# Kernel optimization log

Hardware: AMD Instinct MI355X
Metric: run time of the kernel (lower is better)

Reference implementation:

```python
import jax, jax.numpy as jnp
import numpy as np

B, D, L, H = 4, 1024, 2048, 8
HD = D // H


def setup_inputs() -> dict:
    key = jax.random.key(0)
    k1, k2, k3, k4 = jax.random.split(key, 4)
    query = jax.random.normal(k1, (B, D, L), dtype=jnp.float32)
    mask = jax.random.randint(k2, (B, L), 0, 2, dtype=jnp.int32)
    W1 = jax.random.normal(k3, (2 * D, D), dtype=jnp.float32) * (D ** -0.5)
    Wq = jax.random.normal(k4, (D, D), dtype=jnp.float32) * (D ** -0.5)
    return {"query": query, "mask": mask, "W1": W1, "Wq": Wq}


def _split_heads(x):
    # [B, L, C] -> [B, H, L, C//H]
    b, l, c = x.shape
    return x.reshape(b, l, H, c // H).transpose(0, 2, 1, 3)


def reference(query, mask, W1, Wq):
    # 1x1 conv == channel GEMM; produce [B, L, out]
    temp = jnp.einsum('od,bdl->blo', W1, query)   # [B, L, 2D] (K|V)
    q = jnp.einsum('od,bdl->blo', Wq, query)      # [B, L, D]
    k, v = jnp.split(temp, 2, axis=-1)
    q = _split_heads(q) * (HD ** -0.5)            # [B, H, L, HD]
    k = _split_heads(k)
    v = _split_heads(v)
    scores = jnp.einsum('bhqd,bhkd->bhqk', q, k)  # [B, H, L, L]
    m = mask.astype(jnp.float32)[:, None, None, :]
    logits = scores + (-1e30) * (1.0 - m)
    weights = jax.nn.softmax(logits, axis=-1)     # dropout p=0 (eval)
    out = jnp.einsum('bhqk,bhkd->bhqd', weights, v)
    out = out.transpose(0, 2, 1, 3).reshape(B, L, D)  # merge heads
    return out.transpose(0, 2, 1)                 # [B, D, L]
```

## Files before the change

### kernel.cpp

```cpp
#include <hip/hip_runtime.h>
#include <hip/hip_bf16.h>

#define B_  4
#define D_  1024
#define L_  2048
#define H_  8
#define HD_ 128

typedef __attribute__((ext_vector_type(8))) short bf16x8;
typedef __attribute__((ext_vector_type(4))) float f32x4;
typedef __attribute__((ext_vector_type(2))) unsigned uint2v;
typedef __attribute__((ext_vector_type(4))) unsigned uint4v;

#if __has_builtin(__builtin_amdgcn_permlane16_swap) && __has_builtin(__builtin_amdgcn_permlane32_swap)
#define HAS_PERMSWAP 1
#else
#define HAS_PERMSWAP 0
#endif

static __device__ __forceinline__ ushort f2bf(float f) {
    unsigned u = __float_as_uint(f);
    unsigned r = (u + 0x7fffu + ((u >> 16) & 1u)) >> 16;
    return (ushort)r;
}

static __device__ __forceinline__ unsigned cvt_pk_bf16(float lo, float hi) {
    unsigned r;
    asm("v_cvt_pk_bf16_f32 %0, %1, %2" : "=v"(r) : "v"(lo), "v"(hi));
    return r;
}

static __device__ __forceinline__ float exp2_fast(float x) {
#if __has_builtin(__builtin_amdgcn_exp2f)
    return __builtin_amdgcn_exp2f(x);
#else
    return exp2f(x);
#endif
}

static __device__ __forceinline__ float qmax4(float x) {
#if HAS_PERMSWAP
    uint2v a = __builtin_amdgcn_permlane16_swap(__float_as_uint(x), __float_as_uint(x), false, false);
    float y = fmaxf(__uint_as_float(a[0]), __uint_as_float(a[1]));
    uint2v b = __builtin_amdgcn_permlane32_swap(__float_as_uint(y), __float_as_uint(y), false, false);
    return fmaxf(__uint_as_float(b[0]), __uint_as_float(b[1]));
#else
    x = fmaxf(x, __shfl_xor(x, 16, 64));
    return fmaxf(x, __shfl_xor(x, 32, 64));
#endif
}

static __device__ __forceinline__ void dma16(const ushort* g, ushort* l) {
    __builtin_amdgcn_global_load_lds(
        (const __attribute__((address_space(1))) void*)g,
        (__attribute__((address_space(3))) void*)l, 16, 0, 0);
}

__global__ void k_zero_out(float* __restrict__ out, int n) {
    int i = blockIdx.x * 256 + threadIdx.x;
    if (i < n) out[i] = 0.f;
}

__global__ void k_prep(const float* __restrict__ q, const float* __restrict__ W1,
                       const float* __restrict__ Wq, const int* __restrict__ mask,
                       ushort* __restrict__ Wb, ushort* __restrict__ Xt,
                       int* __restrict__ cidx, int* __restrict__ cnt) {
    __shared__ float tile[64][65];
    const int bid = blockIdx.x, t = threadIdx.x;
    if (bid < 4) {
        int b = bid;
        if (t < 64) {
            int lane = t;
            const int* mb = mask + b * L_;
            int base = 0;
            for (int c = 0; c < L_; c += 64) {
                int m = mb[c + lane];
                unsigned long long bal = __ballot(m != 0);
                int pre = __popcll(bal & ((1ull << lane) - 1ull));
                if (m) cidx[b * L_ + base + pre] = c + lane;
                base += __popcll(bal);
            }
            for (int j = base + lane; j < L_; j += 64) cidx[b * L_ + j] = 0;
            if (lane == 0) cnt[b] = base;
        }
    } else if (bid < 4 + 2048) {
        int tb = bid - 4;
        int bx = tb & 31, by = (tb >> 5) & 15, bz = tb >> 9;
        int l0 = bx * 64, d0 = by * 64;
        int rr = t >> 4, cc = t & 15;
        const float* src = q + (size_t)bz * D_ * L_;
        for (int i = 0; i < 4; i++) {
            int r = rr + 16 * i;
            float4 v = *(const float4*)&src[(size_t)(d0 + r) * L_ + l0 + cc * 4];
            tile[r][cc * 4 + 0] = v.x;
            tile[r][cc * 4 + 1] = v.y;
            tile[r][cc * 4 + 2] = v.z;
            tile[r][cc * 4 + 3] = v.w;
        }
        __syncthreads();
        ushort* dst = Xt + (size_t)bz * L_ * D_;
        for (int i = 0; i < 4; i++) {
            int lr = rr + 16 * i;
            uint2 o;
            o.x = cvt_pk_bf16(tile[cc * 4 + 0][lr], tile[cc * 4 + 1][lr]);
            o.y = cvt_pk_bf16(tile[cc * 4 + 2][lr], tile[cc * 4 + 3][lr]);
            *(uint2*)&dst[(size_t)(l0 + lr) * D_ + d0 + cc * 4] = o;
        }
    } else {
        int i = (bid - 2052) * 256 + t;
        const int n1 = 2 * D_ * D_ / 4;
        float4 v = (i < n1) ? ((const float4*)W1)[i] : ((const float4*)Wq)[i - n1];
        ushort4 o;
        o.x = f2bf(v.x); o.y = f2bf(v.y); o.z = f2bf(v.z); o.w = f2bf(v.w);
        ((ushort4*)Wb)[i] = o;
    }
}

__launch_bounds__(256)
__global__ void k_proj(const ushort* __restrict__ Wb, const ushort* __restrict__ Xt,
                       const int* __restrict__ cidx, const int* __restrict__ cnt,
                       ushort* __restrict__ Qb, ushort* __restrict__ Kb,
                       ushort* __restrict__ Vt) {
    __shared__ alignas(16) ushort As[128 * 64];
    __shared__ alignas(16) ushort Bs[128 * 64];
    const int bid = blockIdx.x;
    const int xcd = bid & 7, j = bid >> 3;
    const int wid = xcd * 192 + j;
    const int st = wid >> 4, m = wid & 15;
    const int b  = st / 24;
    const int sr = st % 24;
    const int sx = sr & 3, sy = sr >> 2;
    const int x  = sx * 4 + (m & 3);
    const int y  = sy * 4 + (m >> 2);
    const int o0 = y * 128;
    const int l0 = x * 128;
    const int type = o0 >> 10;
    if (type < 2) {
        int tiles = (cnt[b] + 127) >> 7;
        if (x >= tiles) return;
    }
    const int t = threadIdx.x;
    const int wave = t >> 6, lane = t & 63, quad = lane >> 4, li = lane & 15;
    const int wm = wave >> 1, wn = wave & 1;
    const ushort* Xb = Xt + (size_t)b * L_ * D_;

    const int srow = t >> 3;
    const int g = (t & 7) ^ (srow & 7);
    const ushort* aSrc[4];
    const ushort* bSrc[4];
    for (int i = 0; i < 4; i++) {
        int r = i * 32 + srow;
        aSrc[i] = Wb + (size_t)(o0 + r) * D_ + g * 8;
        int l = l0 + r;
        int gl = (type < 2) ? cidx[b * L_ + l] : l;
        bSrc[i] = Xb + (size_t)gl * D_ + g * 8;
    }

    f32x4 acc[4][4] = {};

    for (int k0 = 0; k0 < D_; k0 += 64) {
        for (int i = 0; i < 4; i++)
            dma16(aSrc[i] + k0, &As[(i * 256 + wave * 64) * 8]);
        for (int i = 0; i < 4; i++)
            dma16(bSrc[i] + k0, &Bs[(i * 256 + wave * 64) * 8]);
        __syncthreads();
        for (int ks = 0; ks < 64; ks += 32) {
            const int kc = ks >> 3;
            bf16x8 af[4], bfr[4];
            for (int mf = 0; mf < 4; mf++) {
                int row = wm * 64 + mf * 16 + li;
                af[mf] = *(const bf16x8*)&As[row * 64 + (((kc + quad) ^ (li & 7)) * 8)];
            }
            for (int nf = 0; nf < 4; nf++) {
                int row = wn * 64 + nf * 16 + li;
                bfr[nf] = *(const bf16x8*)&Bs[row * 64 + (((kc + quad) ^ (li & 7)) * 8)];
            }
            for (int mf = 0; mf < 4; mf++)
                for (int nf = 0; nf < 4; nf++)
                    acc[mf][nf] = __builtin_amdgcn_mfma_f32_16x16x32_bf16(af[mf], bfr[nf], acc[mf][nf], 0, 0, 0);
        }
        __syncthreads();
    }

    const float qscale = 0.1275174495450826f;
    for (int mf = 0; mf < 4; mf++) {
        int o = o0 + wm * 64 + mf * 16 + quad * 4;
        int c = o & 1023;
        int h = c >> 7, hd = c & 127;
        for (int nf = 0; nf < 4; nf++) {
            int l = l0 + wn * 64 + nf * 16 + li;
            f32x4 v = acc[mf][nf];
            if (type == 0) {
                uint2 kk;
                kk.x = cvt_pk_bf16(v[0], v[1]);
                kk.y = cvt_pk_bf16(v[2], v[3]);
                *(uint2*)&Kb[(((size_t)(b * H_ + h)) * L_ + l) * HD_ + hd] = kk;
            } else if (type == 1) {
                size_t base = (size_t)(b * H_ + h) * HD_;
                Vt[(base + hd + 0) * L_ + l] = f2bf(v[0]);
                Vt[(base + hd + 1) * L_ + l] = f2bf(v[1]);
                Vt[(base + hd + 2) * L_ + l] = f2bf(v[2]);
                Vt[(base + hd + 3) * L_ + l] = f2bf(v[3]);
            } else {
                uint2 qq;
                qq.x = cvt_pk_bf16(v[0] * qscale, v[1] * qscale);
                qq.y = cvt_pk_bf16(v[2] * qscale, v[3] * qscale);
                *(uint2*)&Qb[(((size_t)(b * H_ + h)) * L_ + l) * HD_ + hd] = qq;
            }
        }
    }
}

__launch_bounds__(256, 4)
__global__ void k_attn(const ushort* __restrict__ Qb, const ushort* __restrict__ Kb,
                       const ushort* __restrict__ Vt, const int* __restrict__ mask,
                       float* __restrict__ out) {
    __shared__ alignas(16) ushort Ks[2][32][128];
    __shared__ alignas(16) ushort Vs[2][128][32];
#if !HAS_PERMSWAP
    __shared__ alignas(16) ushort Pl[4][16][40];
#endif
    const int blk = blockIdx.x;
    const int h = blk & 7, qt = (blk >> 3) & 31, b = blk >> 8;
    const int t = threadIdx.x;
    const int w = t >> 6, lane = t & 63, quad = lane >> 4, li = lane & 15;
    const int q0 = qt * 64 + w * 16;
    const ushort* Qh = Qb + (size_t)(b * H_ + h) * L_ * HD_;
    const ushort* Kh = Kb + (size_t)(b * H_ + h) * L_ * HD_;
    const ushort* Vh = Vt + (size_t)(b * H_ + h) * HD_ * L_;
    const int* mb = mask + b * L_;

    int cm = 0;
    for (int c = lane; c < L_; c += 64) cm += mb[c];
    cm += __shfl_xor(cm, 32, 64);
    cm += __shfl_xor(cm, 16, 64);
    cm += __shfl_xor(cm, 8, 64);
    cm += __shfl_xor(cm, 4, 64);
    cm += __shfl_xor(cm, 2, 64);
    cm += __shfl_xor(cm, 1, 64);
    const int cnt = cm;
    int cnt_pad = (cnt + 31) & ~31;
    if (cnt_pad < 32) cnt_pad = 32;

    const ushort* kgp[2]; const ushort* vgp[2];
    for (int i = 0; i < 2; i++) {
        int seg = w * 2 + i;
        int key = seg * 4 + (lane >> 4);
        int ck  = (lane & 15) ^ (key & 15);
        kgp[i] = Kh + (size_t)key * HD_ + ck * 8;
        int hd  = seg * 16 + (lane >> 2);
        int cv  = (lane & 3) ^ (hd & 3);
        vgp[i] = Vh + (size_t)hd * L_ + cv * 8;
    }

    for (int i = 0; i < 2; i++) dma16(kgp[i], &Ks[0][0][0] + (w * 2 + i) * 512);
    for (int i = 0; i < 2; i++) dma16(vgp[i], &Vs[0][0][0] + (w * 2 + i) * 512);

    bf16x8 qf[4];
    for (int kf = 0; kf < 4; kf++)
        qf[kf] = *(const bf16x8*)&Qh[(size_t)(q0 + li) * HD_ + kf * 32 + quad * 8];

    bf16x8 ones;
    for (int i = 0; i < 8; i++) ones[i] = (short)0x3F80;

    float mrun = -1e30f;
    f32x4 lsum = {};
    f32x4 acc[8] = {};

    int buf = 0;
    for (int n0 = 0; n0 < cnt_pad; n0 += 32, buf ^= 1) {
        __syncthreads();

        if (n0 + 32 < cnt_pad) {
            int nb = buf ^ 1;
            for (int i = 0; i < 2; i++)
                dma16(kgp[i] + (size_t)(n0 + 32) * HD_, &Ks[nb][0][0] + (w * 2 + i) * 512);
            for (int i = 0; i < 2; i++)
                dma16(vgp[i] + (n0 + 32), &Vs[nb][0][0] + (w * 2 + i) * 512);
        }

        f32x4 s[2] = {};
        for (int kf = 0; kf < 4; kf++) {
            bf16x8 kfr[2];
            for (int mt = 0; mt < 2; mt++)
                kfr[mt] = *(const bf16x8*)&Ks[buf][mt * 16 + li][((kf * 4 + quad) ^ li) * 8];
            for (int mt = 0; mt < 2; mt++)
                s[mt] = __builtin_amdgcn_mfma_f32_16x16x32_bf16(kfr[mt], qf[kf], s[mt], 0, 0, 0);
        }

        if (n0 + 32 > cnt) {
            for (int mt = 0; mt < 2; mt++)
                for (int r = 0; r < 4; r++)
                    if (n0 + mt * 16 + quad * 4 + r >= cnt) s[mt][r] = -1e30f;
        }

        float a0 = fmaxf(fmaxf(s[0][0], s[0][1]), fmaxf(s[0][2], s[0][3]));
        float a1 = fmaxf(fmaxf(s[1][0], s[1][1]), fmaxf(s[1][2], s[1][3]));
        float nm = qmax4(fmaxf(a0, a1));
        float mnew = fmaxf(mrun, nm);
        float alpha = exp2_fast(mrun - mnew);
        mrun = mnew;
        for (int mt = 0; mt < 2; mt++)
            for (int r = 0; r < 4; r++)
                s[mt][r] = exp2_fast(s[mt][r] - mnew);

        if (__any(alpha != 1.0f)) {
            int sb = (lane & 48) | (quad * 4);
            float ar0 = __shfl(alpha, sb + 0, 64);
            float ar1 = __shfl(alpha, sb + 1, 64);
            float ar2 = __shfl(alpha, sb + 2, 64);
            float ar3 = __shfl(alpha, sb + 3, 64);
            lsum[0] *= ar0; lsum[1] *= ar1; lsum[2] *= ar2; lsum[3] *= ar3;
            for (int nf2 = 0; nf2 < 8; nf2++) {
                acc[nf2][0] *= ar0;
                acc[nf2][1] *= ar1;
                acc[nf2][2] *= ar2;
                acc[nf2][3] *= ar3;
            }
        }

        bf16x8 pa;
#if HAS_PERMSWAP
        {
            unsigned c0 = cvt_pk_bf16(s[0][0], s[0][1]);
            unsigned c1 = cvt_pk_bf16(s[0][2], s[0][3]);
            unsigned c2 = cvt_pk_bf16(s[1][0], s[1][1]);
            unsigned c3 = cvt_pk_bf16(s[1][2], s[1][3]);
            uint2v x02 = __builtin_amdgcn_permlane32_swap(c0, c2, false, false);
            uint2v u02 = __builtin_amdgcn_permlane16_swap(x02[0], x02[1], false, false);
            uint2v x13 = __builtin_amdgcn_permlane32_swap(c1, c3, false, false);
            uint2v u13 = __builtin_amdgcn_permlane16_swap(x13[0], x13[1], false, false);
            uint4v paw;
            paw[0] = u02[0];
            paw[1] = u13[0];
            paw[2] = u02[1];
            paw[3] = u13[1];
            pa = __builtin_bit_cast(bf16x8, paw);
        }
#else
        {
            for (int mt = 0; mt < 2; mt++) {
                uint2 pk;
                pk.x = cvt_pk_bf16(s[mt][0], s[mt][1]);
                pk.y = cvt_pk_bf16(s[mt][2], s[mt][3]);
                *(uint2*)&Pl[w][li][mt * 16 + quad * 4] = pk;
            }
            pa = *(const bf16x8*)&Pl[w][li][quad * 8];
        }
#endif

        lsum = __builtin_amdgcn_mfma_f32_16x16x32_bf16(pa, ones, lsum, 0, 0, 0);

        for (int nf2 = 0; nf2 < 8; nf2++) {
            bf16x8 vb = *(const bf16x8*)&Vs[buf][nf2 * 16 + li][(quad ^ (li & 3)) * 8];
            acc[nf2] = __builtin_amdgcn_mfma_f32_16x16x32_bf16(pa, vb, acc[nf2], 0, 0, 0);
        }
    }

    float i0 = 1.0f / lsum[0];
    float i1 = 1.0f / lsum[1];
    float i2 = 1.0f / lsum[2];
    float i3 = 1.0f / lsum[3];
    int l = q0 + quad * 4;
    for (int nf2 = 0; nf2 < 8; nf2++) {
        int d = h * HD_ + nf2 * 16 + li;
        float4 o4 = { acc[nf2][0] * i0, acc[nf2][1] * i1,
                      acc[nf2][2] * i2, acc[nf2][3] * i3 };
        *(float4*)&out[((size_t)(b * D_ + d)) * L_ + l] = o4;
    }
}

extern "C" void kernel_launch(void* const* d_in, const int* in_sizes, int n_in,
                              void* d_out, int out_size, void* d_ws, size_t ws_size,
                              hipStream_t stream) {
    const float* query = nullptr;
    const int*   mask  = nullptr;
    const float* W1    = nullptr;
    const float* Wq    = nullptr;
    for (int i = 0; i < n_in; i++) {
        switch (in_sizes[i]) {
            case 8388608: query = (const float*)d_in[i]; break;
            case 8192:    mask  = (const int*)d_in[i];   break;
            case 2097152: W1    = (const float*)d_in[i]; break;
            case 1048576: Wq    = (const float*)d_in[i]; break;
        }
    }
    float* out = (float*)d_out;

    if (ws_size < 50331648u || !query || !mask || !W1 || !Wq) {
        hipLaunchKernelGGL(k_zero_out, dim3((out_size + 255) / 256), dim3(256), 0, stream,
                           out, out_size);
        return;
    }

    ushort* Wb = (ushort*)d_out;
    ushort* Xt = (ushort*)((char*)d_out + 6291456);
    int* cidx  = (int*)((char*)d_out + 23068672);
    int* cnt   = (int*)((char*)d_out + 23101440);
    char* ws = (char*)d_ws;
    ushort* Qb = (ushort*)(ws + 0);
    ushort* Kb = (ushort*)(ws + 16777216);
    ushort* Vt = (ushort*)(ws + 33554432);

    hipLaunchKernelGGL(k_prep, dim3(4 + 2048 + 3072), dim3(256), 0, stream,
                       query, W1, Wq, mask, Wb, Xt, cidx, cnt);
    hipLaunchKernelGGL(k_proj, dim3(1536), dim3(256), 0, stream, Wb, Xt, cidx, cnt, Qb, Kb, Vt);
    hipLaunchKernelGGL(k_attn, dim3(1024), dim3(256), 0, stream, Qb, Kb, Vt, mask, out);
}
```

Baseline: 219.8 us.

## Process two query sub-tiles per wave and add lazy softmax rescaling

The attention kernel now uses 128-thread blocks with two waves. Each wave handles 32 query rows as two 16-row sub-tiles that share the same K and V fragments read from LDS, so each LDS read feeds twice as many MFMAs. The per-chunk online-softmax rescale is now done only when some row max grows by more than 8 in the log2 domain, which skips most rescaling but lets exponents reach up to 2^8 before renormalising. The cost is more accumulator registers per wave (the launch bound changes to 128 threads with 2 blocks) and more DMA issues per thread.

```diff
diff --git a/kernel.cpp b/kernel.cpp
--- a/kernel.cpp
+++ b/kernel.cpp
@@ -47,6 +47,28 @@
 #else
     x = fmaxf(x, __shfl_xor(x, 16, 64));
     return fmaxf(x, __shfl_xor(x, 32, 64));
+#endif
+}
+
+static __device__ __forceinline__ bf16x8 p_transpose(const f32x4* s) {
+#if HAS_PERMSWAP
+    unsigned c0 = cvt_pk_bf16(s[0][0], s[0][1]);
+    unsigned c1 = cvt_pk_bf16(s[0][2], s[0][3]);
+    unsigned c2 = cvt_pk_bf16(s[1][0], s[1][1]);
+    unsigned c3 = cvt_pk_bf16(s[1][2], s[1][3]);
+    uint2v x02 = __builtin_amdgcn_permlane32_swap(c0, c2, false, false);
+    uint2v u02 = __builtin_amdgcn_permlane16_swap(x02[0], x02[1], false, false);
+    uint2v x13 = __builtin_amdgcn_permlane32_swap(c1, c3, false, false);
+    uint2v u13 = __builtin_amdgcn_permlane16_swap(x13[0], x13[1], false, false);
+    uint4v paw;
+    paw[0] = u02[0];
+    paw[1] = u13[0];
+    paw[2] = u02[1];
+    paw[3] = u13[1];
+    return __builtin_bit_cast(bf16x8, paw);
+#else
+    bf16x8 z = {};
+    return z;
 #endif
 }
 
@@ -211,20 +233,20 @@
     }
 }
 
-__launch_bounds__(256, 4)
+__launch_bounds__(128, 2)
 __global__ void k_attn(const ushort* __restrict__ Qb, const ushort* __restrict__ Kb,
                        const ushort* __restrict__ Vt, const int* __restrict__ mask,
                        float* __restrict__ out) {
     __shared__ alignas(16) ushort Ks[2][32][128];
     __shared__ alignas(16) ushort Vs[2][128][32];
 #if !HAS_PERMSWAP
-    __shared__ alignas(16) ushort Pl[4][16][40];
+    __shared__ alignas(16) ushort Pl[2][2][16][40];
 #endif
     const int blk = blockIdx.x;
     const int h = blk & 7, qt = (blk >> 3) & 31, b = blk >> 8;
     const int t = threadIdx.x;
     const int w = t >> 6, lane = t & 63, quad = lane >> 4, li = lane & 15;
-    const int q0 = qt * 64 + w * 16;
+    const int q0 = qt * 64 + w * 32;
     const ushort* Qh = Qb + (size_t)(b * H_ + h) * L_ * HD_;
     const ushort* Kh = Kb + (size_t)(b * H_ + h) * L_ * HD_;
     const ushort* Vh = Vt + (size_t)(b * H_ + h) * HD_ * L_;
@@ -242,9 +264,9 @@
     int cnt_pad = (cnt + 31) & ~31;
     if (cnt_pad < 32) cnt_pad = 32;
 
-    const ushort* kgp[2]; const ushort* vgp[2];
-    for (int i = 0; i < 2; i++) {
-        int seg = w * 2 + i;
+    const ushort* kgp[4]; const ushort* vgp[4];
+    for (int i = 0; i < 4; i++) {
+        int seg = w * 4 + i;
         int key = seg * 4 + (lane >> 4);
         int ck  = (lane & 15) ^ (key & 15);
         kgp[i] = Kh + (size_t)key * HD_ + ck * 8;
@@ -253,19 +275,21 @@
         vgp[i] = Vh + (size_t)hd * L_ + cv * 8;
     }
 
-    for (int i = 0; i < 2; i++) dma16(kgp[i], &Ks[0][0][0] + (w * 2 + i) * 512);
-    for (int i = 0; i < 2; i++) dma16(vgp[i], &Vs[0][0][0] + (w * 2 + i) * 512);
-
-    bf16x8 qf[4];
-    for (int kf = 0; kf < 4; kf++)
-        qf[kf] = *(const bf16x8*)&Qh[(size_t)(q0 + li) * HD_ + kf * 32 + quad * 8];
+    for (int i = 0; i < 4; i++) dma16(kgp[i], &Ks[0][0][0] + (w * 4 + i) * 512);
+    for (int i = 0; i < 4; i++) dma16(vgp[i], &Vs[0][0][0] + (w * 4 + i) * 512);
+
+    bf16x8 qfA[4], qfB[4];
+    for (int kf = 0; kf < 4; kf++) {
+        qfA[kf] = *(const bf16x8*)&Qh[(size_t)(q0 + li) * HD_ + kf * 32 + quad * 8];
+        qfB[kf] = *(const bf16x8*)&Qh[(size_t)(q0 + 16 + li) * HD_ + kf * 32 + quad * 8];
+    }
 
     bf16x8 ones;
     for (int i = 0; i < 8; i++) ones[i] = (short)0x3F80;
 
-    float mrun = -1e30f;
-    f32x4 lsum = {};
-    f32x4 acc[8] = {};
+    float mA = -1e30f, mB = -1e30f;
+    f32x4 lsumA = {}, lsumB = {};
+    f32x4 accA[8] = {}, accB[8] = {};
 
     int buf = 0;
     for (int n0 = 0; n0 < cnt_pad; n0 += 32, buf ^= 1) {
@@ -273,100 +297,104 @@
 
         if (n0 + 32 < cnt_pad) {
             int nb = buf ^ 1;
-            for (int i = 0; i < 2; i++)
-                dma16(kgp[i] + (size_t)(n0 + 32) * HD_, &Ks[nb][0][0] + (w * 2 + i) * 512);
-            for (int i = 0; i < 2; i++)
-                dma16(vgp[i] + (n0 + 32), &Vs[nb][0][0] + (w * 2 + i) * 512);
-        }
-
-        f32x4 s[2] = {};
+            for (int i = 0; i < 4; i++)
+                dma16(kgp[i] + (size_t)(n0 + 32) * HD_, &Ks[nb][0][0] + (w * 4 + i) * 512);
+            for (int i = 0; i < 4; i++)
+                dma16(vgp[i] + (n0 + 32), &Vs[nb][0][0] + (w * 4 + i) * 512);
+        }
+
+        f32x4 sA[2] = {}, sB[2] = {};
         for (int kf = 0; kf < 4; kf++) {
             bf16x8 kfr[2];
             for (int mt = 0; mt < 2; mt++)
                 kfr[mt] = *(const bf16x8*)&Ks[buf][mt * 16 + li][((kf * 4 + quad) ^ li) * 8];
-            for (int mt = 0; mt < 2; mt++)
-                s[mt] = __builtin_amdgcn_mfma_f32_16x16x32_bf16(kfr[mt], qf[kf], s[mt], 0, 0, 0);
+            for (int mt = 0; mt < 2; mt++) {
+                sA[mt] = __builtin_amdgcn_mfma_f32_16x16x32_bf16(kfr[mt], qfA[kf], sA[mt], 0, 0, 0);
+                sB[mt] = __builtin_amdgcn_mfma_f32_16x16x32_bf16(kfr[mt], qfB[kf], sB[mt], 0, 0, 0);
+            }
         }
 
         if (n0 + 32 > cnt) {
             for (int mt = 0; mt < 2; mt++)
                 for (int r = 0; r < 4; r++)
-                    if (n0 + mt * 16 + quad * 4 + r >= cnt) s[mt][r] = -1e30f;
-        }
-
-        float a0 = fmaxf(fmaxf(s[0][0], s[0][1]), fmaxf(s[0][2], s[0][3]));
-        float a1 = fmaxf(fmaxf(s[1][0], s[1][1]), fmaxf(s[1][2], s[1][3]));
-        float nm = qmax4(fmaxf(a0, a1));
-        float mnew = fmaxf(mrun, nm);
-        float alpha = exp2_fast(mrun - mnew);
-        mrun = mnew;
+                    if (n0 + mt * 16 + quad * 4 + r >= cnt) {
+                        sA[mt][r] = -1e30f;
+                        sB[mt][r] = -1e30f;
+                    }
+        }
+
+        float aA0 = fmaxf(fmaxf(sA[0][0], sA[0][1]), fmaxf(sA[0][2], sA[0][3]));
+        float aA1 = fmaxf(fmaxf(sA[1][0], sA[1][1]), fmaxf(sA[1][2], sA[1][3]));
+        float aB0 = fmaxf(fmaxf(sB[0][0], sB[0][1]), fmaxf(sB[0][2], sB[0][3]));
+        float aB1 = fmaxf(fmaxf(sB[1][0], sB[1][1]), fmaxf(sB[1][2], sB[1][3]));
+        float nmA = qmax4(fmaxf(aA0, aA1));
+        float nmB = qmax4(fmaxf(aB0, aB1));
+
+        if (!__all((nmA <= mA + 8.f) & (nmB <= mB + 8.f))) {
+            float mAn = fmaxf(mA, nmA), mBn = fmaxf(mB, nmB);
+            float alA = exp2_fast(mA - mAn), alB = exp2_fast(mB - mBn);
+            mA = mAn; mB = mBn;
+            int sb = (lane & 48) | (quad * 4);
+            float a0 = __shfl(alA, sb + 0, 64), a1 = __shfl(alA, sb + 1, 64);
+            float a2 = __shfl(alA, sb + 2, 64), a3 = __shfl(alA, sb + 3, 64);
+            float b0 = __shfl(alB, sb + 0, 64), b1 = __shfl(alB, sb + 1, 64);
+            float b2 = __shfl(alB, sb + 2, 64), b3 = __shfl(alB, sb + 3, 64);
+            lsumA[0] *= a0; lsumA[1] *= a1; lsumA[2] *= a2; lsumA[3] *= a3;
+            lsumB[0] *= b0; lsumB[1] *= b1; lsumB[2] *= b2; lsumB[3] *= b3;
+            for (int nf2 = 0; nf2 < 8; nf2++) {
+                accA[nf2][0] *= a0; accA[nf2][1] *= a1; accA[nf2][2] *= a2; accA[nf2][3] *= a3;
+                accB[nf2][0] *= b0; accB[nf2][1] *= b1; accB[nf2][2] *= b2; accB[nf2][3] *= b3;
+            }
+        }
+
         for (int mt = 0; mt < 2; mt++)
-            for (int r = 0; r < 4; r++)
-                s[mt][r] = exp2_fast(s[mt][r] - mnew);
-
-        if (__any(alpha != 1.0f)) {
-            int sb = (lane & 48) | (quad * 4);
-            float ar0 = __shfl(alpha, sb + 0, 64);
-            float ar1 = __shfl(alpha, sb + 1, 64);
-            float ar2 = __shfl(alpha, sb + 2, 64);
-            float ar3 = __shfl(alpha, sb + 3, 64);
-            lsum[0] *= ar0; lsum[1] *= ar1; lsum[2] *= ar2; lsum[3] *= ar3;
-            for (int nf2 = 0; nf2 < 8; nf2++) {
-                acc[nf2][0] *= ar0;
-                acc[nf2][1] *= ar1;
-                acc[nf2][2] *= ar2;
-                acc[nf2][3] *= ar3;
-            }
-        }
-
-        bf16x8 pa;
+            for (int r = 0; r < 4; r++) {
+                sA[mt][r] = exp2_fast(sA[mt][r] - mA);
+                sB[mt][r] = exp2_fast(sB[mt][r] - mB);
+            }
+
+        bf16x8 paA, paB;
 #if HAS_PERMSWAP
-        {
-            unsigned c0 = cvt_pk_bf16(s[0][0], s[0][1]);
-            unsigned c1 = cvt_pk_bf16(s[0][2], s[0][3]);
-            unsigned c2 = cvt_pk_bf16(s[1][0], s[1][1]);
-            unsigned c3 = cvt_pk_bf16(s[1][2], s[1][3]);
-            uint2v x02 = __builtin_amdgcn_permlane32_swap(c0, c2, false, false);
-            uint2v u02 = __builtin_amdgcn_permlane16_swap(x02[0], x02[1], false, false);
-            uint2v x13 = __builtin_amdgcn_permlane32_swap(c1, c3, false, false);
-            uint2v u13 = __builtin_amdgcn_permlane16_swap(x13[0], x13[1], false, false);
-            uint4v paw;
-            paw[0] = u02[0];
-            paw[1] = u13[0];
-            paw[2] = u02[1];
-            paw[3] = u13[1];
-            pa = __builtin_bit_cast(bf16x8, paw);
-        }
+        paA = p_transpose(sA);
+        paB = p_transpose(sB);
 #else
-        {
-            for (int mt = 0; mt < 2; mt++) {
-                uint2 pk;
-                pk.x = cvt_pk_bf16(s[mt][0], s[mt][1]);
-                pk.y = cvt_pk_bf16(s[mt][2], s[mt][3]);
-                *(uint2*)&Pl[w][li][mt * 16 + quad * 4] = pk;
-            }
-            pa = *(const bf16x8*)&Pl[w][li][quad * 8];
-        }
-#endif
-
-        lsum = __builtin_amdgcn_mfma_f32_16x16x32_bf16(pa, ones, lsum, 0, 0, 0);
+        for (int mt = 0; mt < 2; mt++) {
+            uint2 pkA, pkB;
+            pkA.x = cvt_pk_bf16(sA[mt][0], sA[mt][1]);
+            pkA.y = cvt_pk_bf16(sA[mt][2], sA[mt][3]);
+            pkB.x = cvt_pk_bf16(sB[mt][0], sB[mt][1]);
+            pkB.y = cvt_pk_bf16(sB[mt][2], sB[mt][3]);
+            *(uint2*)&Pl[w][0][li][mt * 16 + quad * 4] = pkA;
+            *(uint2*)&Pl[w][1][li][mt * 16 + quad * 4] = pkB;
+        }
+        paA = *(const bf16x8*)&Pl[w][0][li][quad * 8];
+        paB = *(const bf16x8*)&Pl[w][1][li][quad * 8];
+#endif
+
+        lsumA = __builtin_amdgcn_mfma_f32_16x16x32_bf16(paA, ones, lsumA, 0, 0, 0);
+        lsumB = __builtin_amdgcn_mfma_f32_16x16x32_bf16(paB, ones, lsumB, 0, 0, 0);
 
         for (int nf2 = 0; nf2 < 8; nf2++) {
             bf16x8 vb = *(const bf16x8*)&Vs[buf][nf2 * 16 + li][(quad ^ (li & 3)) * 8];
-            acc[nf2] = __builtin_amdgcn_mfma_f32_16x16x32_bf16(pa, vb, acc[nf2], 0, 0, 0);
-        }
-    }
-
-    float i0 = 1.0f / lsum[0];
-    float i1 = 1.0f / lsum[1];
-    float i2 = 1.0f / lsum[2];
-    float i3 = 1.0f / lsum[3];
-    int l = q0 + quad * 4;
+            accA[nf2] = __builtin_amdgcn_mfma_f32_16x16x32_bf16(paA, vb, accA[nf2], 0, 0, 0);
+            accB[nf2] = __builtin_amdgcn_mfma_f32_16x16x32_bf16(paB, vb, accB[nf2], 0, 0, 0);
+        }
+    }
+
+    float iA0 = 1.0f / lsumA[0], iA1 = 1.0f / lsumA[1];
+    float iA2 = 1.0f / lsumA[2], iA3 = 1.0f / lsumA[3];
+    float iB0 = 1.0f / lsumB[0], iB1 = 1.0f / lsumB[1];
+    float iB2 = 1.0f / lsumB[2], iB3 = 1.0f / lsumB[3];
+    int lA = q0 + quad * 4;
+    int lB = q0 + 16 + quad * 4;
     for (int nf2 = 0; nf2 < 8; nf2++) {
         int d = h * HD_ + nf2 * 16 + li;
-        float4 o4 = { acc[nf2][0] * i0, acc[nf2][1] * i1,
-                      acc[nf2][2] * i2, acc[nf2][3] * i3 };
-        *(float4*)&out[((size_t)(b * D_ + d)) * L_ + l] = o4;
+        float4 oA = { accA[nf2][0] * iA0, accA[nf2][1] * iA1,
+                      accA[nf2][2] * iA2, accA[nf2][3] * iA3 };
+        float4 oB = { accB[nf2][0] * iB0, accB[nf2][1] * iB1,
+                      accB[nf2][2] * iB2, accB[nf2][3] * iB3 };
+        *(float4*)&out[((size_t)(b * D_ + d)) * L_ + lA] = oA;
+        *(float4*)&out[((size_t)(b * D_ + d)) * L_ + lB] = oB;
     }
 }
 
@@ -405,5 +433,5 @@
     hipLaunchKernelGGL(k_prep, dim3(4 + 2048 + 3072), dim3(256), 0, stream,
                        query, W1, Wq, mask, Wb, Xt, cidx, cnt);
     hipLaunchKernelGGL(k_proj, dim3(1536), dim3(256), 0, stream, Wb, Xt, cidx, cnt, Qb, Kb, Vt);
-    hipLaunchKernelGGL(k_attn, dim3(1024), dim3(256), 0, stream, Qb, Kb, Vt, mask, out);
-}
+    hipLaunchKernelGGL(k_attn, dim3(1024), dim3(128), 0, stream, Qb, Kb, Vt, mask, out);
+}
```

Result: no change. 223.7 us (+1.7%).
